# Kernel optimization log

Measured on AMD Instinct MI355X. Metric: run time of the kernel, lower is better.

The kernel has to match this reference:

```python
import jax, jax.numpy as jnp
import numpy as np

N = 50000
E = 800000
F_IN = 64
HID = 64


def setup_inputs() -> dict:
    key = jax.random.key(0)
    k1, k2, k3, k4, k5, k6 = jax.random.split(key, 6)
    x = jax.random.normal(k1, (N, F_IN), dtype=jnp.float32)
    edge_index = jax.random.randint(k2, (2, E), 0, N, dtype=jnp.int64)
    # GraphSAGE mean-aggregator layers: Linear(2*in -> out) applied to [x || mean_agg(x)]
    W1 = jax.random.normal(k3, (2 * F_IN, HID), dtype=jnp.float32) / np.sqrt(2 * F_IN)
    b1 = jnp.zeros((HID,), dtype=jnp.float32)
    W2 = jax.random.normal(k4, (2 * HID, HID), dtype=jnp.float32) / np.sqrt(2 * HID)
    b2 = jnp.zeros((HID,), dtype=jnp.float32)
    return {"x": x, "edge_index": edge_index, "W1": W1, "b1": b1, "W2": W2, "b2": b2}


def _sage_conv(x, src, dst, W, b):
    # mean aggregation of neighbor (src) features at dst, then linear on [self || agg]
    msg = x[src]                                                   # [E, d] gather
    s = jax.ops.segment_sum(msg, dst, num_segments=N)              # [N, d]
    cnt = jax.ops.segment_sum(jnp.ones((src.shape[0], 1), x.dtype), dst, num_segments=N)
    agg = s / jnp.maximum(cnt, 1.0)
    return jnp.concatenate([x, agg], axis=-1) @ W + b


def reference(x, edge_index, W1, b1, W2, b2):
    src, dst = edge_index[0], edge_index[1]
    h = _sage_conv(x, src, dst, W1, b1)
    h = jax.nn.relu(h)  # dropout is identity at inference
    h = _sage_conv(h, src, dst, W2, b2)
    return h
```

## Files before the change

### kernel.cpp

```cpp
#include <hip/hip_runtime.h>

#define N_NODES 50000
#define N_EDGES 800000
#define F 64
#define CHUNK 3072
#define NWG1 ((N_EDGES + CHUNK - 1) / CHUNK)
#define NBUCK 196
#define BSTRIDE 8192
#define NWTILE (N_NODES / 16)

typedef __attribute__((ext_vector_type(8))) _Float16 half8;
typedef __attribute__((ext_vector_type(4))) float f32x4;
typedef __attribute__((ext_vector_type(8))) unsigned short ushort8v;

__global__ __launch_bounds__(256) void partition_conv(
    const int*    __restrict__ src, const int* __restrict__ dst,
    const float4* __restrict__ xin,
    half8*        __restrict__ x16,
    const float*  __restrict__ W1, const float* __restrict__ W2,
    _Float16*     __restrict__ Wt1, _Float16* __restrict__ Wt2,
    unsigned*     __restrict__ bcur,
    unsigned*     __restrict__ ebuf) {
  int t = threadIdx.x, b = blockIdx.x;
  if (b == NWG1) {
    for (int i = t; i < 64 * 128; i += 256) {
      int n = i >> 7, k = i & 127;
      Wt1[i] = (_Float16)W1[k * 64 + n];
      Wt2[i] = (_Float16)W2[k * 64 + n];
    }
    return;
  }
  __shared__ int hist[256], lscan[256], lcur[256], gbase[256];
  __shared__ unsigned stage[CHUNK];
  hist[t] = 0; __syncthreads();
  int e0 = b * CHUNK;
  int cnt = N_EDGES - e0; if (cnt > CHUNK) cnt = CHUNK;
  for (int i = t; i < cnt; i += 256) atomicAdd(&hist[dst[e0 + i] >> 8], 1);

  const int TOT = N_NODES * F / 8;
  for (int i = b * 256 + t; i < TOT; i += NWG1 * 256) {
    float4 a = xin[i * 2], c = xin[i * 2 + 1];
    half8 hh;
    hh[0] = (_Float16)a.x; hh[1] = (_Float16)a.y;
    hh[2] = (_Float16)a.z; hh[3] = (_Float16)a.w;
    hh[4] = (_Float16)c.x; hh[5] = (_Float16)c.y;
    hh[6] = (_Float16)c.z; hh[7] = (_Float16)c.w;
    x16[i] = hh;
  }
  __syncthreads();

  int v = hist[t];
  lscan[t] = v; __syncthreads();
  for (int off = 1; off < 256; off <<= 1) {
    int a = (t >= off) ? lscan[t - off] : 0;
    __syncthreads();
    lscan[t] += a;
    __syncthreads();
  }
  lscan[t] -= v;
  lcur[t] = lscan[t];
  if (v > 0) gbase[t] = (int)atomicAdd(&bcur[t], (unsigned)v);
  __syncthreads();

  for (int i = t; i < cnt; i += 256) {
    int d = dst[e0 + i], s = src[e0 + i];
    int bb = d >> 8;
    int p = atomicAdd(&lcur[bb], 1);
    stage[p] = ((unsigned)bb << 24) | ((unsigned)(d & 255) << 16) | (unsigned)s;
  }
  __syncthreads();
  for (int i = t; i < cnt; i += 256) {
    unsigned e = stage[i];
    int bb = e >> 24;
    ebuf[bb * BSTRIDE + gbase[bb] + (i - lscan[bb])] = e;
  }
}

__global__ __launch_bounds__(256) void bucket_sort(
    const unsigned* __restrict__ ebuf, const unsigned* __restrict__ bcur,
    unsigned short* __restrict__ edge_src, int* __restrict__ row_start,
    int* __restrict__ deg) {
  __shared__ int lhist[128], lscan[128], lcur[128];
  __shared__ unsigned short srt[BSTRIDE / 2];
  int B = blockIdx.x, t = threadIdx.x;
  int b = B >> 1, h = B & 1;
  int s0 = b * BSTRIDE;
  int cnt = (int)bcur[b];

  if (t < 128) lhist[t] = 0;
  __syncthreads();
  for (int i = t; i < cnt; i += 256) {
    int bin = (int)((ebuf[s0 + i] >> 16) & 255);
    if ((bin >> 7) == h) atomicAdd(&lhist[bin & 127], 1);
  }
  __syncthreads();

  int v  = (t < 128) ? lhist[t] : 0;
  int pv = (v + 7) & ~7;
  if (t < 128) lscan[t] = pv;
  __syncthreads();
  for (int off = 1; off < 128; off <<= 1) {
    int a = (t >= off && t < 128) ? lscan[t - off] : 0;
    __syncthreads();
    if (t < 128) lscan[t] += a;
    __syncthreads();
  }
  if (t < 128) { lscan[t] -= pv; lcur[t] = lscan[t]; }
  __syncthreads();

  int total_p = lscan[127] + ((lhist[127] + 7) & ~7);
  int base    = h * (BSTRIDE / 2);

  for (int i = t; i < cnt; i += 256) {
    unsigned e = ebuf[s0 + i];
    int bin = (int)((e >> 16) & 255);
    if ((bin >> 7) == h) {
      int p = atomicAdd(&lcur[bin & 127], 1);
      srt[p] = (unsigned short)(e & 0xFFFFu);
    }
  }
  __syncthreads();
  if (t < 128) {
    int p0 = lscan[t];
    for (int j = v; j < pv; ++j) srt[p0 + j] = 0;
  }
  __syncthreads();

  for (int i = t; i < total_p; i += 256) edge_src[s0 + base + i] = srt[i];

  if (t < 128) {
    int n = b * 256 + h * 128 + t;
    if (n < N_NODES) { row_start[n] = s0 + base + lscan[t]; deg[n] = v; }
  }
}

__global__ __launch_bounds__(256) void sage_layer_fused(
    const half8*    __restrict__ feat16,
    const _Float16* __restrict__ self16,
    const int*      __restrict__ row_start,
    const int*      __restrict__ deg,
    const unsigned short* __restrict__ edge_src,
    const _Float16* __restrict__ Wt,
    const float*    __restrict__ bias,
    float*          __restrict__ outf,
    unsigned short* __restrict__ out16,
    int do_relu) {
  __shared__ _Float16 lmean[32 * 72];
  int t = threadIdx.x;
  int w = t >> 6, lane = t & 63;

  {
    int o = lane >> 3, q = lane & 7;
    int n = blockIdx.x * 32 + w * 8 + o;
    if (n < N_NODES) {
      int start = row_start[n];
      int d     = deg[n];
      half8 acc8 = (half8){0, 0, 0, 0, 0, 0, 0, 0};
      if (d > 0) {
        const ushort8v* idp = (const ushort8v*)(edge_src + start);
        int nb = (d + 15) >> 4;
        ushort8v iA = idp[0], iB = idp[1];
        for (int b = 0; b < nb; ++b) {
          half8 h0 = feat16[(size_t)iA[0] * 8 + q];
          half8 h1 = feat16[(size_t)iA[1] * 8 + q];
          half8 h2 = feat16[(size_t)iA[2] * 8 + q];
          half8 h3 = feat16[(size_t)iA[3] * 8 + q];
          half8 h4 = feat16[(size_t)iA[4] * 8 + q];
          half8 h5 = feat16[(size_t)iA[5] * 8 + q];
          half8 h6 = feat16[(size_t)iA[6] * 8 + q];
          half8 h7 = feat16[(size_t)iA[7] * 8 + q];
          half8 h8 = feat16[(size_t)iB[0] * 8 + q];
          half8 h9 = feat16[(size_t)iB[1] * 8 + q];
          half8 hA = feat16[(size_t)iB[2] * 8 + q];
          half8 hB = feat16[(size_t)iB[3] * 8 + q];
          half8 hC = feat16[(size_t)iB[4] * 8 + q];
          half8 hD = feat16[(size_t)iB[5] * 8 + q];
          half8 hE = feat16[(size_t)iB[6] * 8 + q];
          half8 hF = feat16[(size_t)iB[7] * 8 + q];
          ushort8v nA, nB;
          if (b + 1 < nb) {
            nA = idp[2 * b + 2];
            nB = idp[2 * b + 3];
          }
          int b0 = b * 16;
          if (b0 + 16 <= d) {
            acc8 += h0; acc8 += h1; acc8 += h2; acc8 += h3;
            acc8 += h4; acc8 += h5; acc8 += h6; acc8 += h7;
            acc8 += h8; acc8 += h9; acc8 += hA; acc8 += hB;
            acc8 += hC; acc8 += hD; acc8 += hE; acc8 += hF;
          } else {
            if (b0 +  0 < d) acc8 += h0;
            if (b0 +  1 < d) acc8 += h1;
            if (b0 +  2 < d) acc8 += h2;
            if (b0 +  3 < d) acc8 += h3;
            if (b0 +  4 < d) acc8 += h4;
            if (b0 +  5 < d) acc8 += h5;
            if (b0 +  6 < d) acc8 += h6;
            if (b0 +  7 < d) acc8 += h7;
            if (b0 +  8 < d) acc8 += h8;
            if (b0 +  9 < d) acc8 += h9;
            if (b0 + 10 < d) acc8 += hA;
            if (b0 + 11 < d) acc8 += hB;
            if (b0 + 12 < d) acc8 += hC;
            if (b0 + 13 < d) acc8 += hD;
            if (b0 + 14 < d) acc8 += hE;
            if (b0 + 15 < d) acc8 += hF;
          }
          if (b + 1 < nb) { iA = nA; iB = nB; }
        }
      }
      float inv = (d > 0) ? 1.0f / (float)d : 0.0f;
      half8 hm;
      #pragma unroll
      for (int k = 0; k < 8; ++k) hm[k] = (_Float16)((float)acc8[k] * inv);
      *(half8*)&lmean[(w * 8 + o) * 72 + q * 8] = hm;
    }
  }
  __syncthreads();

  int tile = w >> 1;
  int wt = blockIdx.x * 2 + tile;
  if (wt >= NWTILE) return;
  int m = lane & 15, quad = lane >> 4;
  size_t arow = (size_t)(wt * 16 + m) * 64 + quad * 8;
  half8 a0 = *(const half8*)(self16 + arow);
  half8 a1 = *(const half8*)(self16 + arow + 32);
  int ln = tile * 16 + m;
  half8 a2 = *(const half8*)&lmean[ln * 72 + quad * 8];
  half8 a3 = *(const half8*)&lmean[ln * 72 + quad * 8 + 32];

  int nt0 = (w & 1) * 2;
  #pragma unroll
  for (int i = 0; i < 2; ++i) {
    int nt = nt0 + i;
    float bv = bias[nt * 16 + m];
    f32x4 acc = (f32x4){bv, bv, bv, bv};
    const _Float16* wrow = Wt + (size_t)(nt * 16 + m) * 128 + quad * 8;
    half8 b0 = *(const half8*)(wrow);
    half8 b1 = *(const half8*)(wrow + 32);
    half8 b2 = *(const half8*)(wrow + 64);
    half8 b3 = *(const half8*)(wrow + 96);
    acc = __builtin_amdgcn_mfma_f32_16x16x32_f16(a0, b0, acc, 0, 0, 0);
    acc = __builtin_amdgcn_mfma_f32_16x16x32_f16(a1, b1, acc, 0, 0, 0);
    acc = __builtin_amdgcn_mfma_f32_16x16x32_f16(a2, b2, acc, 0, 0, 0);
    acc = __builtin_amdgcn_mfma_f32_16x16x32_f16(a3, b3, acc, 0, 0, 0);
    #pragma unroll
    for (int r = 0; r < 4; ++r) {
      size_t off = (size_t)(wt * 16 + quad * 4 + r) * 64 + nt * 16 + m;
      float v = acc[r];
      if (do_relu) v = fmaxf(v, 0.0f);
      if (outf)  outf[off] = v;
      if (out16) { _Float16 hv = (_Float16)v; out16[off] = *(unsigned short*)&hv; }
    }
  }
}

extern "C" void kernel_launch(void* const* d_in, const int* in_sizes, int n_in,
                              void* d_out, int out_size, void* d_ws, size_t ws_size,
                              hipStream_t stream) {
  const float* x  = (const float*)d_in[0];
  const int*   ei = (const int*)d_in[1];
  const float* W1 = (const float*)d_in[2];
  const float* b1 = (const float*)d_in[3];
  const float* W2 = (const float*)d_in[4];
  const float* b2 = (const float*)d_in[5];
  float* out = (float*)d_out;

  const int* src = ei;
  const int* dst = ei + N_EDGES;

  int* wsi       = (int*)d_ws;
  unsigned* bcur = (unsigned*)wsi;
  int* deg       = wsi + 256;
  int* row_start = wsi + 50304;
  unsigned short* edge_src = (unsigned short*)(wsi + 100352);
  unsigned* ebuf = (unsigned*)(wsi + 903168);
  half8* x16     = (half8*)(wsi + 2508800);
  unsigned short* h116 = (unsigned short*)(wsi + 4108800);
  _Float16* Wt1  = (_Float16*)(wsi + 5708800);
  _Float16* Wt2  = (_Float16*)(wsi + 5712896);

  hipMemsetAsync(bcur, 0, 256 * sizeof(unsigned), stream);

  dim3 blk(256);
  partition_conv<<<NWG1 + 1, blk, 0, stream>>>(
      src, dst, (const float4*)x, x16, W1, W2, Wt1, Wt2, bcur, ebuf);
  bucket_sort<<<NBUCK * 2, blk, 0, stream>>>(ebuf, bcur, edge_src, row_start, deg);

  dim3 grd_fused((N_NODES + 31) / 32);

  sage_layer_fused<<<grd_fused, blk, 0, stream>>>(
      x16, (const _Float16*)x16, row_start, deg, edge_src,
      Wt1, b1, nullptr, h116, 1);
  sage_layer_fused<<<grd_fused, blk, 0, stream>>>(
      (const half8*)h116, (const _Float16*)h116, row_start, deg, edge_src,
      Wt2, b2, out, nullptr, 0);
}
```

Baseline: 148.3 us.

## Merge all four kernels into one cooperative persistent kernel with grid syncs

```diff
diff --git a/kernel.cpp b/kernel.cpp
--- a/kernel.cpp
+++ b/kernel.cpp
@@ -1,4 +1,7 @@
 #include <hip/hip_runtime.h>
+#include <hip/hip_cooperative_groups.h>
+
+namespace cg = cooperative_groups;
 
 #define N_NODES 50000
 #define N_EDGES 800000
@@ -8,133 +11,13 @@
 #define NBUCK 196
 #define BSTRIDE 8192
 #define NWTILE (N_NODES / 16)
+#define NTILE2 ((N_NODES + 31) / 32)
 
 typedef __attribute__((ext_vector_type(8))) _Float16 half8;
 typedef __attribute__((ext_vector_type(4))) float f32x4;
 typedef __attribute__((ext_vector_type(8))) unsigned short ushort8v;
 
-__global__ __launch_bounds__(256) void partition_conv(
-    const int*    __restrict__ src, const int* __restrict__ dst,
-    const float4* __restrict__ xin,
-    half8*        __restrict__ x16,
-    const float*  __restrict__ W1, const float* __restrict__ W2,
-    _Float16*     __restrict__ Wt1, _Float16* __restrict__ Wt2,
-    unsigned*     __restrict__ bcur,
-    unsigned*     __restrict__ ebuf) {
-  int t = threadIdx.x, b = blockIdx.x;
-  if (b == NWG1) {
-    for (int i = t; i < 64 * 128; i += 256) {
-      int n = i >> 7, k = i & 127;
-      Wt1[i] = (_Float16)W1[k * 64 + n];
-      Wt2[i] = (_Float16)W2[k * 64 + n];
-    }
-    return;
-  }
-  __shared__ int hist[256], lscan[256], lcur[256], gbase[256];
-  __shared__ unsigned stage[CHUNK];
-  hist[t] = 0; __syncthreads();
-  int e0 = b * CHUNK;
-  int cnt = N_EDGES - e0; if (cnt > CHUNK) cnt = CHUNK;
-  for (int i = t; i < cnt; i += 256) atomicAdd(&hist[dst[e0 + i] >> 8], 1);
-
-  const int TOT = N_NODES * F / 8;
-  for (int i = b * 256 + t; i < TOT; i += NWG1 * 256) {
-    float4 a = xin[i * 2], c = xin[i * 2 + 1];
-    half8 hh;
-    hh[0] = (_Float16)a.x; hh[1] = (_Float16)a.y;
-    hh[2] = (_Float16)a.z; hh[3] = (_Float16)a.w;
-    hh[4] = (_Float16)c.x; hh[5] = (_Float16)c.y;
-    hh[6] = (_Float16)c.z; hh[7] = (_Float16)c.w;
-    x16[i] = hh;
-  }
-  __syncthreads();
-
-  int v = hist[t];
-  lscan[t] = v; __syncthreads();
-  for (int off = 1; off < 256; off <<= 1) {
-    int a = (t >= off) ? lscan[t - off] : 0;
-    __syncthreads();
-    lscan[t] += a;
-    __syncthreads();
-  }
-  lscan[t] -= v;
-  lcur[t] = lscan[t];
-  if (v > 0) gbase[t] = (int)atomicAdd(&bcur[t], (unsigned)v);
-  __syncthreads();
-
-  for (int i = t; i < cnt; i += 256) {
-    int d = dst[e0 + i], s = src[e0 + i];
-    int bb = d >> 8;
-    int p = atomicAdd(&lcur[bb], 1);
-    stage[p] = ((unsigned)bb << 24) | ((unsigned)(d & 255) << 16) | (unsigned)s;
-  }
-  __syncthreads();
-  for (int i = t; i < cnt; i += 256) {
-    unsigned e = stage[i];
-    int bb = e >> 24;
-    ebuf[bb * BSTRIDE + gbase[bb] + (i - lscan[bb])] = e;
-  }
-}
-
-__global__ __launch_bounds__(256) void bucket_sort(
-    const unsigned* __restrict__ ebuf, const unsigned* __restrict__ bcur,
-    unsigned short* __restrict__ edge_src, int* __restrict__ row_start,
-    int* __restrict__ deg) {
-  __shared__ int lhist[128], lscan[128], lcur[128];
-  __shared__ unsigned short srt[BSTRIDE / 2];
-  int B = blockIdx.x, t = threadIdx.x;
-  int b = B >> 1, h = B & 1;
-  int s0 = b * BSTRIDE;
-  int cnt = (int)bcur[b];
-
-  if (t < 128) lhist[t] = 0;
-  __syncthreads();
-  for (int i = t; i < cnt; i += 256) {
-    int bin = (int)((ebuf[s0 + i] >> 16) & 255);
-    if ((bin >> 7) == h) atomicAdd(&lhist[bin & 127], 1);
-  }
-  __syncthreads();
-
-  int v  = (t < 128) ? lhist[t] : 0;
-  int pv = (v + 7) & ~7;
-  if (t < 128) lscan[t] = pv;
-  __syncthreads();
-  for (int off = 1; off < 128; off <<= 1) {
-    int a = (t >= off && t < 128) ? lscan[t - off] : 0;
-    __syncthreads();
-    if (t < 128) lscan[t] += a;
-    __syncthreads();
-  }
-  if (t < 128) { lscan[t] -= pv; lcur[t] = lscan[t]; }
-  __syncthreads();
-
-  int total_p = lscan[127] + ((lhist[127] + 7) & ~7);
-  int base    = h * (BSTRIDE / 2);
-
-  for (int i = t; i < cnt; i += 256) {
-    unsigned e = ebuf[s0 + i];
-    int bin = (int)((e >> 16) & 255);
-    if ((bin >> 7) == h) {
-      int p = atomicAdd(&lcur[bin & 127], 1);
-      srt[p] = (unsigned short)(e & 0xFFFFu);
-    }
-  }
-  __syncthreads();
-  if (t < 128) {
-    int p0 = lscan[t];
-    for (int j = v; j < pv; ++j) srt[p0 + j] = 0;
-  }
-  __syncthreads();
-
-  for (int i = t; i < total_p; i += 256) edge_src[s0 + base + i] = srt[i];
-
-  if (t < 128) {
-    int n = b * 256 + h * 128 + t;
-    if (n < N_NODES) { row_start[n] = s0 + base + lscan[t]; deg[n] = v; }
-  }
-}
-
-__global__ __launch_bounds__(256) void sage_layer_fused(
+__device__ __forceinline__ void sage_layer_phase(
     const half8*    __restrict__ feat16,
     const _Float16* __restrict__ self16,
     const int*      __restrict__ row_start,
@@ -144,14 +27,14 @@
     const float*    __restrict__ bias,
     float*          __restrict__ outf,
     unsigned short* __restrict__ out16,
-    int do_relu) {
-  __shared__ _Float16 lmean[32 * 72];
+    int do_relu, _Float16* lmean, int nblk) {
   int t = threadIdx.x;
   int w = t >> 6, lane = t & 63;
-
-  {
-    int o = lane >> 3, q = lane & 7;
-    int n = blockIdx.x * 32 + w * 8 + o;
+  int o = lane >> 3, q = lane & 7;
+  int m = lane & 15, quad = lane >> 4;
+  for (int vb = blockIdx.x; vb < NTILE2; vb += nblk) {
+    __syncthreads();
+    int n = vb * 32 + w * 8 + o;
     if (n < N_NODES) {
       int start = row_start[n];
       int d     = deg[n];
@@ -215,44 +98,185 @@
       for (int k = 0; k < 8; ++k) hm[k] = (_Float16)((float)acc8[k] * inv);
       *(half8*)&lmean[(w * 8 + o) * 72 + q * 8] = hm;
     }
-  }
-  __syncthreads();
-
-  int tile = w >> 1;
-  int wt = blockIdx.x * 2 + tile;
-  if (wt >= NWTILE) return;
-  int m = lane & 15, quad = lane >> 4;
-  size_t arow = (size_t)(wt * 16 + m) * 64 + quad * 8;
-  half8 a0 = *(const half8*)(self16 + arow);
-  half8 a1 = *(const half8*)(self16 + arow + 32);
-  int ln = tile * 16 + m;
-  half8 a2 = *(const half8*)&lmean[ln * 72 + quad * 8];
-  half8 a3 = *(const half8*)&lmean[ln * 72 + quad * 8 + 32];
-
-  int nt0 = (w & 1) * 2;
-  #pragma unroll
-  for (int i = 0; i < 2; ++i) {
-    int nt = nt0 + i;
-    float bv = bias[nt * 16 + m];
-    f32x4 acc = (f32x4){bv, bv, bv, bv};
-    const _Float16* wrow = Wt + (size_t)(nt * 16 + m) * 128 + quad * 8;
-    half8 b0 = *(const half8*)(wrow);
-    half8 b1 = *(const half8*)(wrow + 32);
-    half8 b2 = *(const half8*)(wrow + 64);
-    half8 b3 = *(const half8*)(wrow + 96);
-    acc = __builtin_amdgcn_mfma_f32_16x16x32_f16(a0, b0, acc, 0, 0, 0);
-    acc = __builtin_amdgcn_mfma_f32_16x16x32_f16(a1, b1, acc, 0, 0, 0);
-    acc = __builtin_amdgcn_mfma_f32_16x16x32_f16(a2, b2, acc, 0, 0, 0);
-    acc = __builtin_amdgcn_mfma_f32_16x16x32_f16(a3, b3, acc, 0, 0, 0);
-    #pragma unroll
-    for (int r = 0; r < 4; ++r) {
-      size_t off = (size_t)(wt * 16 + quad * 4 + r) * 64 + nt * 16 + m;
-      float v = acc[r];
-      if (do_relu) v = fmaxf(v, 0.0f);
-      if (outf)  outf[off] = v;
-      if (out16) { _Float16 hv = (_Float16)v; out16[off] = *(unsigned short*)&hv; }
-    }
-  }
+    __syncthreads();
+    int tile = w >> 1;
+    int wt = vb * 2 + tile;
+    if (wt < NWTILE) {
+      size_t arow = (size_t)(wt * 16 + m) * 64 + quad * 8;
+      half8 a0 = *(const half8*)(self16 + arow);
+      half8 a1 = *(const half8*)(self16 + arow + 32);
+      int ln = tile * 16 + m;
+      half8 a2 = *(const half8*)&lmean[ln * 72 + quad * 8];
+      half8 a3 = *(const half8*)&lmean[ln * 72 + quad * 8 + 32];
+      int nt0 = (w & 1) * 2;
+      #pragma unroll
+      for (int i = 0; i < 2; ++i) {
+        int nt = nt0 + i;
+        float bv = bias[nt * 16 + m];
+        f32x4 acc = (f32x4){bv, bv, bv, bv};
+        const _Float16* wrow = Wt + (size_t)(nt * 16 + m) * 128 + quad * 8;
+        half8 b0 = *(const half8*)(wrow);
+        half8 b1 = *(const half8*)(wrow + 32);
+        half8 b2 = *(const half8*)(wrow + 64);
+        half8 b3 = *(const half8*)(wrow + 96);
+        acc = __builtin_amdgcn_mfma_f32_16x16x32_f16(a0, b0, acc, 0, 0, 0);
+        acc = __builtin_amdgcn_mfma_f32_16x16x32_f16(a1, b1, acc, 0, 0, 0);
+        acc = __builtin_amdgcn_mfma_f32_16x16x32_f16(a2, b2, acc, 0, 0, 0);
+        acc = __builtin_amdgcn_mfma_f32_16x16x32_f16(a3, b3, acc, 0, 0, 0);
+        #pragma unroll
+        for (int r = 0; r < 4; ++r) {
+          size_t off = (size_t)(wt * 16 + quad * 4 + r) * 64 + nt * 16 + m;
+          float v = acc[r];
+          if (do_relu) v = fmaxf(v, 0.0f);
+          if (outf)  outf[off] = v;
+          if (out16) { _Float16 hv = (_Float16)v; out16[off] = *(unsigned short*)&hv; }
+        }
+      }
+    }
+  }
+}
+
+__global__ __launch_bounds__(256) void sage_mega(
+    const int*    __restrict__ src, const int* __restrict__ dst,
+    const float4* __restrict__ xin, half8* __restrict__ x16,
+    const float*  __restrict__ W1, const float* __restrict__ W2,
+    _Float16*     __restrict__ Wt1, _Float16* __restrict__ Wt2,
+    unsigned*     __restrict__ bcur, unsigned* __restrict__ ebuf,
+    unsigned short* __restrict__ edge_src, int* __restrict__ row_start,
+    int*          __restrict__ deg, unsigned short* __restrict__ h116,
+    const float*  __restrict__ b1, const float* __restrict__ b2,
+    float*        __restrict__ out) {
+  cg::grid_group grid = cg::this_grid();
+  int t = threadIdx.x;
+  int nblk = gridDim.x;
+
+  __shared__ int hist[256], lscan[256], lcur[256], gbase[256];
+  __shared__ unsigned stage[CHUNK];
+  __shared__ int k2h[128], k2s[128], k2c[128];
+  __shared__ unsigned short srt[BSTRIDE / 2];
+  __shared__ _Float16 lmean[32 * 72];
+
+  const int TOT = N_NODES * F / 8;
+  for (int i = blockIdx.x * 256 + t; i < TOT; i += nblk * 256) {
+    float4 a = xin[i * 2], c = xin[i * 2 + 1];
+    half8 hh;
+    hh[0] = (_Float16)a.x; hh[1] = (_Float16)a.y;
+    hh[2] = (_Float16)a.z; hh[3] = (_Float16)a.w;
+    hh[4] = (_Float16)c.x; hh[5] = (_Float16)c.y;
+    hh[6] = (_Float16)c.z; hh[7] = (_Float16)c.w;
+    x16[i] = hh;
+  }
+
+  for (int b = blockIdx.x; b <= NWG1; b += nblk) {
+    if (b == NWG1) {
+      for (int i = t; i < 64 * 128; i += 256) {
+        int n = i >> 7, k = i & 127;
+        Wt1[i] = (_Float16)W1[k * 64 + n];
+        Wt2[i] = (_Float16)W2[k * 64 + n];
+      }
+      continue;
+    }
+    hist[t] = 0; __syncthreads();
+    int e0 = b * CHUNK;
+    int cnt = N_EDGES - e0; if (cnt > CHUNK) cnt = CHUNK;
+    for (int i = t; i < cnt; i += 256) atomicAdd(&hist[dst[e0 + i] >> 8], 1);
+    __syncthreads();
+
+    int v = hist[t];
+    lscan[t] = v; __syncthreads();
+    for (int off = 1; off < 256; off <<= 1) {
+      int a = (t >= off) ? lscan[t - off] : 0;
+      __syncthreads();
+      lscan[t] += a;
+      __syncthreads();
+    }
+    lscan[t] -= v;
+    lcur[t] = lscan[t];
+    if (v > 0) gbase[t] = (int)atomicAdd(&bcur[t], (unsigned)v);
+    __syncthreads();
+
+    for (int i = t; i < cnt; i += 256) {
+      int d = dst[e0 + i], s = src[e0 + i];
+      int bb = d >> 8;
+      int p = atomicAdd(&lcur[bb], 1);
+      stage[p] = ((unsigned)bb << 24) | ((unsigned)(d & 255) << 16) | (unsigned)s;
+    }
+    __syncthreads();
+    for (int i = t; i < cnt; i += 256) {
+      unsigned e = stage[i];
+      int bb = e >> 24;
+      ebuf[bb * BSTRIDE + gbase[bb] + (i - lscan[bb])] = e;
+    }
+    __syncthreads();
+  }
+
+  __threadfence();
+  grid.sync();
+
+  for (int B = blockIdx.x; B < NBUCK * 2; B += nblk) {
+    int b = B >> 1, h = B & 1;
+    int s0 = b * BSTRIDE;
+    int cnt = (int)bcur[b];
+
+    if (t < 128) k2h[t] = 0;
+    __syncthreads();
+    for (int i = t; i < cnt; i += 256) {
+      int bin = (int)((ebuf[s0 + i] >> 16) & 255);
+      if ((bin >> 7) == h) atomicAdd(&k2h[bin & 127], 1);
+    }
+    __syncthreads();
+
+    int v  = (t < 128) ? k2h[t] : 0;
+    int pv = (v + 7) & ~7;
+    if (t < 128) k2s[t] = pv;
+    __syncthreads();
+    for (int off = 1; off < 128; off <<= 1) {
+      int a = (t >= off && t < 128) ? k2s[t - off] : 0;
+      __syncthreads();
+      if (t < 128) k2s[t] += a;
+      __syncthreads();
+    }
+    if (t < 128) { k2s[t] -= pv; k2c[t] = k2s[t]; }
+    __syncthreads();
+
+    int total_p = k2s[127] + ((k2h[127] + 7) & ~7);
+    int base    = h * (BSTRIDE / 2);
+
+    for (int i = t; i < cnt; i += 256) {
+      unsigned e = ebuf[s0 + i];
+      int bin = (int)((e >> 16) & 255);
+      if ((bin >> 7) == h) {
+        int p = atomicAdd(&k2c[bin & 127], 1);
+        srt[p] = (unsigned short)(e & 0xFFFFu);
+      }
+    }
+    __syncthreads();
+    if (t < 128) {
+      int p0 = k2s[t];
+      for (int j = v; j < pv; ++j) srt[p0 + j] = 0;
+    }
+    __syncthreads();
+
+    for (int i = t; i < total_p; i += 256) edge_src[s0 + base + i] = srt[i];
+
+    if (t < 128) {
+      int n = b * 256 + h * 128 + t;
+      if (n < N_NODES) { row_start[n] = s0 + base + k2s[t]; deg[n] = v; }
+    }
+    __syncthreads();
+  }
+
+  __threadfence();
+  grid.sync();
+
+  sage_layer_phase(x16, (const _Float16*)x16, row_start, deg, edge_src,
+                   Wt1, b1, nullptr, h116, 1, lmean, nblk);
+
+  __threadfence();
+  grid.sync();
+
+  sage_layer_phase((const half8*)h116, (const _Float16*)h116, row_start, deg,
+                   edge_src, Wt2, b2, out, nullptr, 0, lmean, nblk);
 }
 
 extern "C" void kernel_launch(void* const* d_in, const int* in_sizes, int n_in,
@@ -282,17 +306,19 @@
 
   hipMemsetAsync(bcur, 0, 256 * sizeof(unsigned), stream);
 
-  dim3 blk(256);
-  partition_conv<<<NWG1 + 1, blk, 0, stream>>>(
-      src, dst, (const float4*)x, x16, W1, W2, Wt1, Wt2, bcur, ebuf);
-  bucket_sort<<<NBUCK * 2, blk, 0, stream>>>(ebuf, bcur, edge_src, row_start, deg);
-
-  dim3 grd_fused((N_NODES + 31) / 32);
-
-  sage_layer_fused<<<grd_fused, blk, 0, stream>>>(
-      x16, (const _Float16*)x16, row_start, deg, edge_src,
-      Wt1, b1, nullptr, h116, 1);
-  sage_layer_fused<<<grd_fused, blk, 0, stream>>>(
-      (const half8*)h116, (const _Float16*)h116, row_start, deg, edge_src,
-      Wt2, b2, out, nullptr, 0);
+  static int nblk = 0;
+  if (nblk == 0) {
+    int bpc = 0;
+    hipError_t e = hipOccupancyMaxActiveBlocksPerMultiprocessor(&bpc, sage_mega, 256, 0);
+    if (e != hipSuccess || bpc < 1) bpc = 1;
+    nblk = bpc * 256;
+    if (nblk > NTILE2) nblk = NTILE2;
+  }
+
+  const float4* xv = (const float4*)x;
+  void* args[] = {(void*)&src, (void*)&dst, (void*)&xv, (void*)&x16,
+                  (void*)&W1, (void*)&W2, (void*)&Wt1, (void*)&Wt2,
+                  (void*)&bcur, (void*)&ebuf, (void*)&edge_src, (void*)&row_start,
+                  (void*)&deg, (void*)&h116, (void*)&b1, (void*)&b2, (void*)&out};
+  hipLaunchCooperativeKernel(sage_mega, dim3(nblk), dim3(256), args, 0, stream);
 }
```

New measurement: 488.5 us. +229.4%, slower.
